# Performance work log

Hardware: AMD Instinct MI355X
Metric: run time of the kernel (lower is better)

Reference implementation:

```python
import jax, jax.numpy as jnp
import numpy as np

# dims: N batch, L seq, H heads, d projection_dim, P position_dimension
N, Lq, Lk, H, d, P = 2, 1024, 1024, 8, 64, 1
D = H * d


def _kernel(x):
    # _log_exp_kernel: positive feature map log(1+exp(x)) (softplus)
    return jax.nn.softplus(x)


def setup_inputs() -> dict:
    key = jax.random.key(0)
    ks = jax.random.split(key, 8)
    sc = 1.0 / np.sqrt(D).astype(np.float32)
    return {
        "query": jax.random.normal(ks[0], (N, Lq, D), jnp.float32),
        "key_seq": jax.random.normal(ks[1], (N, Lk, D), jnp.float32),
        "Wq": jax.random.normal(ks[2], (D, D), jnp.float32) * sc,
        "Wk": jax.random.normal(ks[3], (D, D), jnp.float32) * sc,
        "Wv": jax.random.normal(ks[4], (D, D), jnp.float32) * sc,
        "position_coeffs": jax.random.uniform(ks[5], (H, d), jnp.float32, 0.5, 1.5),
        "position_weight": jax.random.normal(ks[6], (H, d, P), jnp.float32) * 1e-3,
        "position_bias": jax.random.normal(ks[7], (H, d), jnp.float32) * 1e-2,
    }


def reference(query, key_seq, Wq, Wk, Wv, position_coeffs, position_weight, position_bias):
    # torch Linear (no bias): y = x @ W.T
    q = _kernel(jnp.einsum('nld,ed->nle', query, Wq).reshape(N, Lq, H, d))
    k = _kernel(jnp.einsum('nld,ed->nle', key_seq, Wk).reshape(N, Lk, H, d))
    v = jnp.einsum('nld,ed->nle', key_seq, Wv).reshape(N, Lk, H, d)
    # (N, H, L, d)
    q = jnp.transpose(q, (0, 2, 1, 3))
    k = jnp.transpose(k, (0, 2, 1, 3))
    v = jnp.transpose(v, (0, 2, 1, 3))

    # default positions: arange, query_offset = 0
    qpos = jnp.broadcast_to(jnp.arange(Lq, dtype=jnp.float32).reshape(1, Lq, 1), (N, Lq, P))
    kpos = jnp.broadcast_to(jnp.arange(Lk, dtype=jnp.float32).reshape(1, Lk, 1), (N, Lk, P))
    pq = jnp.einsum('nlp,hkp->nhlk', qpos, position_weight) + position_bias[None, :, None, :]
    pk = jnp.einsum('nlp,hkp->nhlk', kpos, position_weight)

    coeff = position_coeffs[None, :, None, :]  # (1, H, 1, d)

    def part(f, values):
        # causal (mask_future) linear attention via inclusive cumsum over keys
        Qf = q * f(pq) * coeff           # (N, H, Lq, d)
        Kf = k * f(pk)                   # (N, H, Lk, d)
        S = jnp.cumsum(jnp.einsum('nhkd,nhke->nhkde', Kf, values), axis=2)
        return jnp.einsum('nhqd,nhqde->nhqe', Qf, S)

    num = part(jnp.cos, v) + part(jnp.sin, v)           # (N, H, Lq, d)
    unit = jnp.ones((N, H, Lk, 1), jnp.float32)
    den = part(jnp.cos, unit) + part(jnp.sin, unit)     # (N, H, Lq, 1)
    attn = num / den
    return jnp.transpose(attn, (0, 2, 1, 3)).reshape(N, Lq, D)
```

## Files before the change

kernel.cpp:

```cpp
#include <hip/hip_runtime.h>
#include <cmath>

#define NB    2
#define LSEQ  1024
#define NH    8
#define HD    64
#define DD    512
#define FDIM  128
#define EV    65
#define SEP   80
#define CHUNK 64
#define NC    16
#define NBH   16

typedef short short8 __attribute__((ext_vector_type(8)));
typedef float floatx4 __attribute__((ext_vector_type(4)));
typedef unsigned short ushort;

__device__ __forceinline__ float softplusf(float x) {
  return fmaxf(x, 0.0f) + log1pf(expf(-fabsf(x)));
}

__device__ __forceinline__ ushort f2bf(float f) {
  unsigned u = __float_as_uint(f);
  u += 0x7fffu + ((u >> 16) & 1u);
  return (ushort)(u >> 16);
}

__device__ __forceinline__ short8 cvt8(float4 a, float4 b) {
  short8 r;
  r[0] = (short)f2bf(a.x); r[1] = (short)f2bf(a.y);
  r[2] = (short)f2bf(a.z); r[3] = (short)f2bf(a.w);
  r[4] = (short)f2bf(b.x); r[5] = (short)f2bf(b.y);
  r[6] = (short)f2bf(b.z); r[7] = (short)f2bf(b.w);
  return r;
}

__global__ __launch_bounds__(256) void k_proj(
    const float* __restrict__ Xq, const float* __restrict__ Xkv,
    const float* __restrict__ Wq, const float* __restrict__ Wk,
    const float* __restrict__ Wv, const float* __restrict__ pw,
    const float* __restrict__ pb, const float* __restrict__ pc,
    ushort* __restrict__ Qfb, ushort* __restrict__ Kfb,
    ushort* __restrict__ Vxb)
{
  __shared__ short Al[2][64][72];
  __shared__ short Bl[2][64][72];
  const int b = blockIdx.x;
  int m0, e0, pmode;
  const float *X, *W;
  if (b < 256) {
    m0 = (b >> 3) << 6; e0 = (b & 7) << 6;
    X = Xq; W = Wq + (size_t)e0 * DD; pmode = 0;
  } else {
    const int bb = b - 256;
    m0 = (bb >> 4) << 6;
    const int nt = bb & 15;
    e0 = (nt & 7) << 6;
    X = Xkv;
    if (nt < 8) { W = Wk + (size_t)e0 * DD; pmode = 1; }
    else        { W = Wv + (size_t)e0 * DD; pmode = 2; }
  }
  const int tid  = threadIdx.x;
  const int r    = tid >> 2;
  const int ko   = (tid & 3) << 4;
  const int wave = tid >> 6, lane = tid & 63;
  const int quad = lane >> 4, lm = lane & 15;
  const float* Ag = X + (size_t)(m0 + r) * DD + ko;
  const float* Bg = W + (size_t)r * DD + ko;
  float4 a[4], bb4[4];
#pragma unroll
  for (int u = 0; u < 4; ++u) {
    a[u]   = *(const float4*)(Ag + (u << 2));
    bb4[u] = *(const float4*)(Bg + (u << 2));
  }
  *(short8*)&Al[0][r][ko]     = cvt8(a[0], a[1]);
  *(short8*)&Al[0][r][ko + 8] = cvt8(a[2], a[3]);
  *(short8*)&Bl[0][r][ko]     = cvt8(bb4[0], bb4[1]);
  *(short8*)&Bl[0][r][ko + 8] = cvt8(bb4[2], bb4[3]);
  __syncthreads();

  floatx4 acc[4] = {};
  for (int k0 = 0; k0 < DD; k0 += 64) {
    const int cur  = (k0 >> 6) & 1;
    const bool more = (k0 + 64 < DD);
    if (more) {
#pragma unroll
      for (int u = 0; u < 4; ++u) {
        a[u]   = *(const float4*)(Ag + k0 + 64 + (u << 2));
        bb4[u] = *(const float4*)(Bg + k0 + 64 + (u << 2));
      }
    }
#pragma unroll
    for (int ks = 0; ks < 2; ++ks) {
      const short8 af = *(const short8*)&Al[cur][(wave << 4) + lm][(quad << 3) + (ks << 5)];
#pragma unroll
      for (int t = 0; t < 4; ++t) {
        const short8 bf = *(const short8*)&Bl[cur][(t << 4) + lm][(quad << 3) + (ks << 5)];
        acc[t] = __builtin_amdgcn_mfma_f32_16x16x32_bf16(af, bf, acc[t], 0, 0, 0);
      }
    }
    if (more) {
      const int nxt = cur ^ 1;
      *(short8*)&Al[nxt][r][ko]     = cvt8(a[0], a[1]);
      *(short8*)&Al[nxt][r][ko + 8] = cvt8(a[2], a[3]);
      *(short8*)&Bl[nxt][r][ko]     = cvt8(bb4[0], bb4[1]);
      *(short8*)&Bl[nxt][r][ko + 8] = cvt8(bb4[2], bb4[3]);
    }
    __syncthreads();
  }
#pragma unroll
  for (int t = 0; t < 4; ++t) {
    const int e = e0 + (t << 4) + lm;
    const int h = e >> 6, jj = e & 63;
    if (pmode == 2) {
#pragma unroll
      for (int rg = 0; rg < 4; ++rg) {
        const int m = m0 + (wave << 4) + (quad << 2) + rg;
        const int n = m >> 10, l = m & 1023;
        Vxb[((size_t)(n * NH + h) * LSEQ + l) * HD + jj] = f2bf(acc[t][rg]);
      }
    } else {
      const float pwv = pw[e];
      const float pbv = (pmode == 0) ? pb[e] : 0.0f;
      const float pcv = (pmode == 0) ? pc[e] : 1.0f;
      ushort* base = (pmode == 0) ? Qfb : Kfb;
#pragma unroll
      for (int rg = 0; rg < 4; ++rg) {
        const int m = m0 + (wave << 4) + (quad << 2) + rg;
        const int n = m >> 10, l = m & 1023;
        const float v = softplusf(acc[t][rg]) * pcv;
        const float ang = fmaf((float)l, pwv, pbv);
        ushort* dst = &base[((size_t)(n * NH + h) * LSEQ + l) * FDIM + jj];
        dst[0]  = f2bf(v * __cosf(ang));
        dst[64] = f2bf(v * __sinf(ang));
      }
    }
  }
}

__global__ __launch_bounds__(256) void k_chunk_sums(
    const ushort* __restrict__ Kfb, const ushort* __restrict__ Vxb,
    float* __restrict__ S)
{
  const int blk = blockIdx.x;
  const int bh  = blk >> 5;
  const int c   = (blk >> 1) & (NC - 1);
  const int fh  = blk & 1;
  const int f0  = fh << 6;
  const int t0  = c * CHUNK;
  const int tid  = threadIdx.x;
  const int wave = tid >> 6, lane = tid & 63;
  const int quad = lane >> 4, lm = lane & 15;

  __shared__ short KT[64][72];
  __shared__ short VT[80][72];

  for (int i = tid; i < 64 * 8; i += 256) {
    const int t = i & 63, f8 = (i >> 6) << 3;
    const short8 k8 = *(const short8*)&Kfb[((size_t)bh * LSEQ + t0 + t) * FDIM + f0 + f8];
#pragma unroll
    for (int u = 0; u < 8; ++u) KT[f8 + u][t] = k8[u];
  }
  for (int i = tid; i < 64 * 8; i += 256) {
    const int t = i & 63, e8 = (i >> 6) << 3;
    const short8 v8 = *(const short8*)&Vxb[((size_t)bh * LSEQ + t0 + t) * HD + e8];
#pragma unroll
    for (int u = 0; u < 8; ++u) VT[e8 + u][t] = v8[u];
  }
  if (tid < CHUNK) VT[64][tid] = (short)0x3F80;
  __syncthreads();

  short8 aK[2];
#pragma unroll
  for (int ks = 0; ks < 2; ++ks)
    aK[ks] = *(const short8*)&KT[(wave << 4) + lm][(quad << 3) + (ks << 5)];
  floatx4 acc[5] = {};
#pragma unroll
  for (int nt = 0; nt < 5; ++nt)
#pragma unroll
    for (int ks = 0; ks < 2; ++ks) {
      const short8 bf = *(const short8*)&VT[(nt << 4) + lm][(quad << 3) + (ks << 5)];
      acc[nt] = __builtin_amdgcn_mfma_f32_16x16x32_bf16(aK[ks], bf, acc[nt], 0, 0, 0);
    }

  float* Sb = &S[(size_t)(bh * NC + c) * SEP * FDIM];
#pragma unroll
  for (int nt = 0; nt < 4; ++nt)
#pragma unroll
    for (int rg = 0; rg < 4; ++rg) {
      const int f = f0 + (wave << 4) + (quad << 2) + rg;
      Sb[((nt << 4) + lm) * FDIM + f] = acc[nt][rg];
    }
  if (lm == 0) {
#pragma unroll
    for (int rg = 0; rg < 4; ++rg) {
      const int f = f0 + (wave << 4) + (quad << 2) + rg;
      Sb[64 * FDIM + f] = acc[4][rg];
    }
  }
}

__global__ __launch_bounds__(256) void k_scan(
    const float* __restrict__ S, ushort* __restrict__ PTb)
{
  const int bh = blockIdx.x / 13;
  const int eg = blockIdx.x % 13;
  const size_t cs = (size_t)SEP * FDIM;
  const float* Sg = S + (size_t)bh * NC * cs;
  ushort* Pg = PTb + (size_t)bh * NC * cs;
  for (int i = threadIdx.x; i < 5 * FDIM; i += 256) {
    const int e = eg * 5 + (i >> 7);
    const int f = i & 127;
    const int off = e * FDIM + f;
    float v[NC];
#pragma unroll
    for (int c = 0; c < NC; ++c) v[c] = Sg[(size_t)c * cs + off];
    float s = 0.0f;
#pragma unroll
    for (int c = 0; c < NC; ++c) {
      Pg[(size_t)c * cs + off] = f2bf(s);
      s += v[c];
    }
  }
}

__global__ __launch_bounds__(256) void k_chunk_out(
    const ushort* __restrict__ Qfb, const ushort* __restrict__ Kfb,
    const ushort* __restrict__ Vxb, const ushort* __restrict__ PTb,
    float* __restrict__ Out)
{
  const int c  = blockIdx.x & (NC - 1);
  const int bh = blockIdx.x >> 4;
  const int n  = bh >> 3, h = bh & 7;
  const int t0 = c * CHUNK;
  const int tid  = threadIdx.x;
  const int wave = tid >> 6, lane = tid & 63;
  const int quad = lane >> 4, lm = lane & 15;

  __shared__ short QL[64][128];
  __shared__ short KL[64][128];
  __shared__ short ScL[64][72];
  __shared__ short PT[80][136];
  __shared__ short VT[80][72];
  __shared__ float DenL[64];

  const ushort* Qg = &Qfb[((size_t)bh * LSEQ + t0) * FDIM];
  const ushort* Kg = &Kfb[((size_t)bh * LSEQ + t0) * FDIM];
  for (int i = tid; i < 64 * 16; i += 256) {
    const int r = i >> 4, f8 = (i & 15) << 3;
    *(short8*)&QL[r][f8] = *(const short8*)&Qg[r * FDIM + f8];
    *(short8*)&KL[r][f8] = *(const short8*)&Kg[r * FDIM + f8];
  }
  {
    const ushort* Pg = &PTb[(size_t)(bh * NC + c) * SEP * FDIM];
    for (int i = tid; i < 65 * 16; i += 256) {
      const int e = i >> 4, f8 = (i & 15) << 3;
      *(short8*)&PT[e][f8] = *(const short8*)&Pg[e * FDIM + f8];
    }
  }
  for (int i = tid; i < 64 * 8; i += 256) {
    const int t = i & 63, e8 = (i >> 6) << 3;
    const short8 v8 = *(const short8*)&Vxb[((size_t)bh * LSEQ + t0 + t) * HD + e8];
#pragma unroll
    for (int u = 0; u < 8; ++u) VT[e8 + u][t] = v8[u];
  }
  if (tid < CHUNK) VT[64][tid] = (short)0x3F80;
  __syncthreads();

  short8 aQ[4];
#pragma unroll
  for (int ks = 0; ks < 4; ++ks)
    aQ[ks] = *(const short8*)&QL[(wave << 4) + lm][(quad << 3) + (ks << 5)];

  floatx4 accS[4] = {};
#pragma unroll
  for (int nt = 0; nt < 4; ++nt)
#pragma unroll
    for (int ks = 0; ks < 4; ++ks) {
      const short8 b = *(const short8*)&KL[(nt << 4) + lm][(quad << 3) + (ks << 5)];
      accS[nt] = __builtin_amdgcn_mfma_f32_16x16x32_bf16(aQ[ks], b, accS[nt], 0, 0, 0);
    }
#pragma unroll
  for (int nt = 0; nt < 4; ++nt)
#pragma unroll
    for (int rg = 0; rg < 4; ++rg) {
      const int m = (wave << 4) + (quad << 2) + rg;
      const int t = (nt << 4) + lm;
      ScL[m][t] = (short)((t <= m) ? f2bf(accS[nt][rg]) : 0);
    }

  floatx4 accN[5] = {};
#pragma unroll
  for (int nt = 0; nt < 5; ++nt)
#pragma unroll
    for (int ks = 0; ks < 4; ++ks) {
      const short8 b = *(const short8*)&PT[(nt << 4) + lm][(quad << 3) + (ks << 5)];
      accN[nt] = __builtin_amdgcn_mfma_f32_16x16x32_bf16(aQ[ks], b, accN[nt], 0, 0, 0);
    }

  short8 aS[2];
#pragma unroll
  for (int ks = 0; ks < 2; ++ks)
    aS[ks] = *(const short8*)&ScL[(wave << 4) + lm][(quad << 3) + (ks << 5)];
  floatx4 accV[5] = {};
#pragma unroll
  for (int nt = 0; nt < 5; ++nt)
#pragma unroll
    for (int ks = 0; ks < 2; ++ks) {
      const short8 b = *(const short8*)&VT[(nt << 4) + lm][(quad << 3) + (ks << 5)];
      accV[nt] = __builtin_amdgcn_mfma_f32_16x16x32_bf16(aS[ks], b, accV[nt], 0, 0, 0);
    }

  if (lm == 0) {
#pragma unroll
    for (int rg = 0; rg < 4; ++rg)
      DenL[(wave << 4) + (quad << 2) + rg] = accN[4][rg] + accV[4][rg];
  }

#pragma unroll
  for (int rg = 0; rg < 4; ++rg) {
    const int m = (wave << 4) + (quad << 2) + rg;
    const float rden = 1.0f / DenL[m];
    const int l = t0 + m;
#pragma unroll
    for (int nt = 0; nt < 4; ++nt) {
      const float val = (accN[nt][rg] + accV[nt][rg]) * rden;
      Out[((size_t)(n * LSEQ + l)) * DD + h * HD + (nt << 4) + lm] = val;
    }
  }
}

extern "C" void kernel_launch(void* const* d_in, const int* in_sizes, int n_in,
                              void* d_out, int out_size, void* d_ws, size_t ws_size,
                              hipStream_t stream) {
  (void)in_sizes; (void)n_in; (void)out_size; (void)ws_size;
  const float* query  = (const float*)d_in[0];
  const float* keyseq = (const float*)d_in[1];
  const float* Wq     = (const float*)d_in[2];
  const float* Wk     = (const float*)d_in[3];
  const float* Wv     = (const float*)d_in[4];
  const float* pc     = (const float*)d_in[5];
  const float* pw     = (const float*)d_in[6];
  const float* pb     = (const float*)d_in[7];
  float* out = (float*)d_out;

  ushort* Qfb = (ushort*)d_ws;
  ushort* Kfb = Qfb + (size_t)NBH * LSEQ * FDIM;
  ushort* Vxb = Kfb + (size_t)NBH * LSEQ * FDIM;
  float*  S   = (float*)(Vxb + (size_t)NBH * LSEQ * HD);
  ushort* PTb = (ushort*)(S + (size_t)NBH * NC * SEP * FDIM);

  k_proj      <<<768,          256, 0, stream>>>(query, keyseq, Wq, Wk, Wv, pw, pb, pc, Qfb, Kfb, Vxb);
  k_chunk_sums<<<NBH * NC * 2, 256, 0, stream>>>(Kfb, Vxb, S);
  k_scan      <<<NBH * 13,     256, 0, stream>>>(S, PTb);
  k_chunk_out <<<NBH * NC,     256, 0, stream>>>(Qfb, Kfb, Vxb, PTb, out);
}
```

Before: 113.2 us.

## Pre-convert inputs and weights to bf16 in a separate kernel before projection

Adds a k_cvt kernel that converts the query, key and weight matrices from fp32 to bf16 once, so k_proj reads half the bytes and no longer repeats the conversion for every tile that shares an operand. k_proj also remaps block indices so that consecutive blocks are spread across the Q, K and V work, and k_chunk_out pads the QL/KL shared arrays to cut LDS bank conflicts. The trade-off is one extra kernel launch plus a full read and write of the inputs into workspace.

```diff
diff --git a/kernel.cpp b/kernel.cpp
--- a/kernel.cpp
+++ b/kernel.cpp
@@ -36,48 +36,68 @@
   return r;
 }
 
-__global__ __launch_bounds__(256) void k_proj(
+__global__ __launch_bounds__(256) void k_cvt(
     const float* __restrict__ Xq, const float* __restrict__ Xkv,
     const float* __restrict__ Wq, const float* __restrict__ Wk,
-    const float* __restrict__ Wv, const float* __restrict__ pw,
-    const float* __restrict__ pb, const float* __restrict__ pc,
+    const float* __restrict__ Wv,
+    ushort* __restrict__ Xqb, ushort* __restrict__ Xkvb,
+    ushort* __restrict__ Wqb, ushort* __restrict__ Wkb,
+    ushort* __restrict__ Wvb)
+{
+  const int i = blockIdx.x * 256 + threadIdx.x;
+  const float* src; ushort* dst; int g;
+  if (i < 131072)      { src = Xq;  dst = Xqb;  g = i; }
+  else if (i < 262144) { src = Xkv; dst = Xkvb; g = i - 131072; }
+  else if (i < 294912) { src = Wq;  dst = Wqb;  g = i - 262144; }
+  else if (i < 327680) { src = Wk;  dst = Wkb;  g = i - 294912; }
+  else                 { src = Wv;  dst = Wvb;  g = i - 327680; }
+  const float4 a = ((const float4*)src)[(size_t)g * 2];
+  const float4 b = ((const float4*)src)[(size_t)g * 2 + 1];
+  *(short8*)&dst[(size_t)g * 8] = cvt8(a, b);
+}
+
+__global__ __launch_bounds__(256) void k_proj(
+    const ushort* __restrict__ Xqb, const ushort* __restrict__ Xkvb,
+    const ushort* __restrict__ Wqb, const ushort* __restrict__ Wkb,
+    const ushort* __restrict__ Wvb,
+    const float* __restrict__ pw, const float* __restrict__ pb,
+    const float* __restrict__ pc,
     ushort* __restrict__ Qfb, ushort* __restrict__ Kfb,
     ushort* __restrict__ Vxb)
 {
   __shared__ short Al[2][64][72];
   __shared__ short Bl[2][64][72];
-  const int b = blockIdx.x;
+  const int b = ((blockIdx.x & 7) * 96) + (blockIdx.x >> 3);
   int m0, e0, pmode;
-  const float *X, *W;
+  const ushort *X, *W;
   if (b < 256) {
     m0 = (b >> 3) << 6; e0 = (b & 7) << 6;
-    X = Xq; W = Wq + (size_t)e0 * DD; pmode = 0;
+    X = Xqb; W = Wqb + (size_t)e0 * DD; pmode = 0;
   } else {
     const int bb = b - 256;
     m0 = (bb >> 4) << 6;
     const int nt = bb & 15;
     e0 = (nt & 7) << 6;
-    X = Xkv;
-    if (nt < 8) { W = Wk + (size_t)e0 * DD; pmode = 1; }
-    else        { W = Wv + (size_t)e0 * DD; pmode = 2; }
+    X = Xkvb;
+    if (nt < 8) { W = Wkb + (size_t)e0 * DD; pmode = 1; }
+    else        { W = Wvb + (size_t)e0 * DD; pmode = 2; }
   }
   const int tid  = threadIdx.x;
   const int r    = tid >> 2;
   const int ko   = (tid & 3) << 4;
   const int wave = tid >> 6, lane = tid & 63;
   const int quad = lane >> 4, lm = lane & 15;
-  const float* Ag = X + (size_t)(m0 + r) * DD + ko;
-  const float* Bg = W + (size_t)r * DD + ko;
-  float4 a[4], bb4[4];
-#pragma unroll
-  for (int u = 0; u < 4; ++u) {
-    a[u]   = *(const float4*)(Ag + (u << 2));
-    bb4[u] = *(const float4*)(Bg + (u << 2));
-  }
-  *(short8*)&Al[0][r][ko]     = cvt8(a[0], a[1]);
-  *(short8*)&Al[0][r][ko + 8] = cvt8(a[2], a[3]);
-  *(short8*)&Bl[0][r][ko]     = cvt8(bb4[0], bb4[1]);
-  *(short8*)&Bl[0][r][ko + 8] = cvt8(bb4[2], bb4[3]);
+  const ushort* Ag = X + (size_t)(m0 + r) * DD + ko;
+  const ushort* Bg = W + (size_t)r * DD + ko;
+
+  short8 a0 = *(const short8*)(Ag);
+  short8 a1 = *(const short8*)(Ag + 8);
+  short8 b0 = *(const short8*)(Bg);
+  short8 b1 = *(const short8*)(Bg + 8);
+  *(short8*)&Al[0][r][ko]     = a0;
+  *(short8*)&Al[0][r][ko + 8] = a1;
+  *(short8*)&Bl[0][r][ko]     = b0;
+  *(short8*)&Bl[0][r][ko + 8] = b1;
   __syncthreads();
 
   floatx4 acc[4] = {};
@@ -85,11 +105,10 @@
     const int cur  = (k0 >> 6) & 1;
     const bool more = (k0 + 64 < DD);
     if (more) {
-#pragma unroll
-      for (int u = 0; u < 4; ++u) {
-        a[u]   = *(const float4*)(Ag + k0 + 64 + (u << 2));
-        bb4[u] = *(const float4*)(Bg + k0 + 64 + (u << 2));
-      }
+      a0 = *(const short8*)(Ag + k0 + 64);
+      a1 = *(const short8*)(Ag + k0 + 72);
+      b0 = *(const short8*)(Bg + k0 + 64);
+      b1 = *(const short8*)(Bg + k0 + 72);
     }
 #pragma unroll
     for (int ks = 0; ks < 2; ++ks) {
@@ -102,10 +121,10 @@
     }
     if (more) {
       const int nxt = cur ^ 1;
-      *(short8*)&Al[nxt][r][ko]     = cvt8(a[0], a[1]);
-      *(short8*)&Al[nxt][r][ko + 8] = cvt8(a[2], a[3]);
-      *(short8*)&Bl[nxt][r][ko]     = cvt8(bb4[0], bb4[1]);
-      *(short8*)&Bl[nxt][r][ko + 8] = cvt8(bb4[2], bb4[3]);
+      *(short8*)&Al[nxt][r][ko]     = a0;
+      *(short8*)&Al[nxt][r][ko + 8] = a1;
+      *(short8*)&Bl[nxt][r][ko]     = b0;
+      *(short8*)&Bl[nxt][r][ko + 8] = b1;
     }
     __syncthreads();
   }
@@ -238,8 +257,8 @@
   const int wave = tid >> 6, lane = tid & 63;
   const int quad = lane >> 4, lm = lane & 15;
 
-  __shared__ short QL[64][128];
-  __shared__ short KL[64][128];
+  __shared__ short QL[64][136];
+  __shared__ short KL[64][136];
   __shared__ short ScL[64][72];
   __shared__ short PT[80][136];
   __shared__ short VT[80][72];
@@ -350,8 +369,14 @@
   ushort* Vxb = Kfb + (size_t)NBH * LSEQ * FDIM;
   float*  S   = (float*)(Vxb + (size_t)NBH * LSEQ * HD);
   ushort* PTb = (ushort*)(S + (size_t)NBH * NC * SEP * FDIM);
-
-  k_proj      <<<768,          256, 0, stream>>>(query, keyseq, Wq, Wk, Wv, pw, pb, pc, Qfb, Kfb, Vxb);
+  ushort* Xqb  = PTb + (size_t)NBH * NC * SEP * FDIM;
+  ushort* Xkvb = Xqb  + (size_t)NB * LSEQ * DD;
+  ushort* Wqb  = Xkvb + (size_t)NB * LSEQ * DD;
+  ushort* Wkb  = Wqb  + (size_t)DD * DD;
+  ushort* Wvb  = Wkb  + (size_t)DD * DD;
+
+  k_cvt       <<<1408,         256, 0, stream>>>(query, keyseq, Wq, Wk, Wv, Xqb, Xkvb, Wqb, Wkb, Wvb);
+  k_proj      <<<768,          256, 0, stream>>>(Xqb, Xkvb, Wqb, Wkb, Wvb, pw, pb, pc, Qfb, Kfb, Vxb);
   k_chunk_sums<<<NBH * NC * 2, 256, 0, stream>>>(Kfb, Vxb, S);
   k_scan      <<<NBH * 13,     256, 0, stream>>>(S, PTb);
   k_chunk_out <<<NBH * NC,     256, 0, stream>>>(Qfb, Kfb, Vxb, PTb, out);
```

Result: no change. 111.0 us (-1.9%).
